# Kernel optimization log

Hardware: AMD Instinct MI355X
Metric: run time of the kernel (lower is better)

The kernel has to match this reference:

```python
import jax, jax.numpy as jnp
import numpy as np

EPS = 1e-6  # flax LayerNorm default

def _layernorm(x, scale, bias):
    mu = jnp.mean(x, axis=-1, keepdims=True)
    var = jnp.mean(jnp.square(x - mu), axis=-1, keepdims=True)
    return (x - mu) * jax.lax.rsqrt(var + EPS) * scale + bias

def _rel_pos_index(ws):
    coords = np.stack(np.meshgrid(np.arange(ws), np.arange(ws), indexing='ij'))  # [2,ws,ws]
    cf = coords.reshape(2, -1)
    rel = (cf[:, :, None] - cf[:, None, :]).transpose(1, 2, 0)  # [N,N,2]
    rel[..., 0] += ws - 1
    rel[..., 1] += ws - 1
    rel[..., 0] *= 2 * ws - 1
    return rel.sum(-1)  # [N,N] in [0,(2ws-1)^2)

def setup_inputs() -> dict:
    key = jax.random.key(0)
    ks = jax.random.split(key, 8)
    B, H, W, C = 16, 56, 56, 384
    L, heads, ws = 2, 12, 7
    s = 0.02
    return {
        'x': jax.random.normal(ks[0], (B, H, W, C), jnp.float32),
        'ln1_s': jnp.ones((L, C), jnp.float32),
        'ln1_b': jnp.zeros((L, C), jnp.float32),
        'qkv_w': jax.random.normal(ks[1], (L, C, 3 * C), jnp.float32) * s,
        'rpb': jax.random.normal(ks[2], (L, (2 * ws - 1) ** 2, heads), jnp.float32) * s,
        'proj_w': jax.random.normal(ks[3], (L, C, C), jnp.float32) * s,
        'ln2_s': jnp.ones((L, C), jnp.float32),
        'ln2_b': jnp.zeros((L, C), jnp.float32),
        'mlp_w1': jax.random.normal(ks[4], (L, C, 4 * C), jnp.float32) * s,
        'mlp_b1': jnp.zeros((L, 4 * C), jnp.float32),
        'mlp_w2': jax.random.normal(ks[5], (L, 4 * C, C), jnp.float32) * s,
        'mlp_b2': jnp.zeros((L, C), jnp.float32),
        'window_size': 7,
    }

def reference(x, ln1_s, ln1_b, qkv_w, rpb, proj_w, ln2_s, ln2_b, mlp_w1, mlp_b1, mlp_w2, mlp_b2, window_size):
    B, H, W, C = x.shape
    ws = int(window_size)
    L = qkv_w.shape[0]
    heads = rpb.shape[-1]
    hd = C // heads
    N = ws * ws
    idx = jnp.asarray(_rel_pos_index(ws))  # [N,N] static

    # --- split to windows: [B,H,W,C] -> [B*nWh*nWw, N, C]
    xw = x.reshape(B, H // ws, ws, W // ws, ws, C)
    xw = xw.transpose(0, 1, 3, 2, 4, 5).reshape(-1, N, C)

    for l in range(L):
        # --- windowed MHSA with relative position bias
        h = _layernorm(xw, ln1_s[l], ln1_b[l])
        qkv = (h @ qkv_w[l]).reshape(-1, N, 3, heads, hd)
        q, k, v = qkv[:, :, 0], qkv[:, :, 1], qkv[:, :, 2]  # [nW,N,heads,hd]
        attn = jnp.einsum('wqhd,wkhd->whqk', q, k) * (hd ** -0.5)
        bias = rpb[l][idx].transpose(2, 0, 1)  # [heads,N,N]
        attn = jax.nn.softmax(attn + bias[None], axis=-1)
        o = jnp.einsum('whqk,wkhd->wqhd', attn, v).reshape(-1, N, C)
        xw = xw + o @ proj_w[l]
        # --- MLP block
        h = _layernorm(xw, ln2_s[l], ln2_b[l])
        h = jax.nn.gelu(h @ mlp_w1[l] + mlp_b1[l])
        xw = xw + (h @ mlp_w2[l] + mlp_b2[l])

    # --- merge windows back to [B,H,W,C]
    out = xw.reshape(B, H // ws, W // ws, ws, ws, C)
    out = out.transpose(0, 1, 3, 2, 4, 5).reshape(B, H, W, C)
    return out
```

## Files before the change

### kernel.cpp

```cpp
#include <hip/hip_runtime.h>
#include <hip/hip_bf16.h>

typedef __bf16 bf16;
typedef __attribute__((ext_vector_type(4))) __bf16 bf16x4;
typedef __attribute__((ext_vector_type(8))) __bf16 bf16x8;
typedef __attribute__((ext_vector_type(4))) float f32x4;

__device__ __forceinline__ void async_ld16(const void* g, void* l) {
    __builtin_amdgcn_global_load_lds(
        (const __attribute__((address_space(1))) unsigned int*)g,
        (__attribute__((address_space(3))) unsigned int*)l, 16, 0, 0);
}

__global__ __launch_bounds__(256) void k_f2bt(const float* __restrict__ in,
                                              bf16* __restrict__ out, int Kd, int Nd) {
    int id = blockIdx.x * 256 + threadIdx.x;
    if (id >= Kd * Nd) return;
    int k = id / Nd, n = id - k * Nd;
    out[(size_t)n * Kd + k] = (bf16)in[id];
}

__global__ __launch_bounds__(256) void k_reorder_in(const float4* __restrict__ x,
                                                    float4* __restrict__ xres) {
    int id = blockIdx.x * 256 + threadIdx.x;
    int c4 = id % 96;
    int t = id / 96;
    int b = t / 3136;
    int rem = t - b * 3136;
    int y = rem / 56;
    int xc = rem - y * 56;
    int w = b * 64 + (y / 7) * 8 + (xc / 7);
    int n = (y % 7) * 7 + (xc % 7);
    xres[(size_t)(w * 49 + n) * 96 + c4] = x[id];
}

__global__ __launch_bounds__(256) void k_reorder_out(const float4* __restrict__ xres,
                                                     float4* __restrict__ out) {
    int id = blockIdx.x * 256 + threadIdx.x;
    int c4 = id % 96;
    int t = id / 96;
    int b = t / 3136;
    int rem = t - b * 3136;
    int y = rem / 56;
    int xc = rem - y * 56;
    int w = b * 64 + (y / 7) * 8 + (xc / 7);
    int n = (y % 7) * 7 + (xc % 7);
    out[id] = xres[(size_t)(w * 49 + n) * 96 + c4];
}

__global__ __launch_bounds__(256) void k_ln(const float* __restrict__ xres,
                                            const float* __restrict__ s,
                                            const float* __restrict__ b,
                                            bf16* __restrict__ h) {
    int t = blockIdx.x * 4 + (threadIdx.x >> 6);
    int lane = threadIdx.x & 63;
    const float4* row = (const float4*)(xres + (size_t)t * 384);
    float4 v0 = row[lane];
    float4 v1 = make_float4(0.f, 0.f, 0.f, 0.f);
    if (lane < 32) v1 = row[64 + lane];
    float sum = v0.x + v0.y + v0.z + v0.w + v1.x + v1.y + v1.z + v1.w;
#pragma unroll
    for (int m = 1; m < 64; m <<= 1) sum += __shfl_xor(sum, m);
    float mu = sum * (1.f / 384.f);
    float sq = (v0.x - mu) * (v0.x - mu) + (v0.y - mu) * (v0.y - mu) +
               (v0.z - mu) * (v0.z - mu) + (v0.w - mu) * (v0.w - mu);
    if (lane < 32)
        sq += (v1.x - mu) * (v1.x - mu) + (v1.y - mu) * (v1.y - mu) +
              (v1.z - mu) * (v1.z - mu) + (v1.w - mu) * (v1.w - mu);
#pragma unroll
    for (int m = 1; m < 64; m <<= 1) sq += __shfl_xor(sq, m);
    float r = rsqrtf(sq * (1.f / 384.f) + 1e-6f);
    const float4* s4 = (const float4*)s;
    const float4* b4 = (const float4*)b;
    bf16* ho = h + (size_t)t * 384;
    {
        float4 sv = s4[lane], bv = b4[lane];
        bf16x4 ov;
        ov[0] = (bf16)((v0.x - mu) * r * sv.x + bv.x);
        ov[1] = (bf16)((v0.y - mu) * r * sv.y + bv.y);
        ov[2] = (bf16)((v0.z - mu) * r * sv.z + bv.z);
        ov[3] = (bf16)((v0.w - mu) * r * sv.w + bv.w);
        *(bf16x4*)&ho[lane * 4] = ov;
    }
    if (lane < 32) {
        float4 sv = s4[64 + lane], bv = b4[64 + lane];
        bf16x4 ov;
        ov[0] = (bf16)((v1.x - mu) * r * sv.x + bv.x);
        ov[1] = (bf16)((v1.y - mu) * r * sv.y + bv.y);
        ov[2] = (bf16)((v1.z - mu) * r * sv.z + bv.z);
        ov[3] = (bf16)((v1.w - mu) * r * sv.w + bv.w);
        *(bf16x4*)&ho[256 + lane * 4] = ov;
    }
}

__device__ inline float gelu_f(float x) {
    float u = 0.7978845608028654f * (x + 0.044715f * x * x * x);
    float t = 1.f - 2.f / (__expf(2.f * u) + 1.f);
    return 0.5f * x * (1.f + t);
}

template <int EPI>
__global__ __launch_bounds__(256) void k_gemm(const bf16* __restrict__ A,
                                              const bf16* __restrict__ Bt,
                                              const float* __restrict__ bias,
                                              float* __restrict__ resid,
                                              bf16* __restrict__ Cout,
                                              int N, int K) {
    __shared__ __align__(16) bf16 As[128 * 64];
    __shared__ __align__(16) bf16 Bs[128 * 64];
    int tid = threadIdx.x;
    int m0 = blockIdx.x * 128;
    int n0 = blockIdx.y * 128;
    int wave = tid >> 6, lane = tid & 63;
    int wm = (wave >> 1) * 64, wn = (wave & 1) * 64;
    int lrow = lane & 15, quad = lane >> 4;

    f32x4 acc[4][4] = {};

    int rsub = lane >> 3;
    int ksl = ((lane & 7) ^ rsub) << 3;
    int rbase = wave * 32 + rsub;
    const bf16* ga = A + (size_t)(m0 + rbase) * K + ksl;
    const bf16* gb = Bt + (size_t)(n0 + rbase) * K + ksl;
    size_t row8 = (size_t)8 * K;
    bf16* lA = &As[wave * 32 * 64];
    bf16* lB = &Bs[wave * 32 * 64];

    for (int kb = 0; kb < K; kb += 64) {
        __syncthreads();
#pragma unroll
        for (int c = 0; c < 4; c++) {
            async_ld16(ga + c * row8 + kb, lA + c * 512);
            async_ld16(gb + c * row8 + kb, lB + c * 512);
        }
        __syncthreads();

        bf16x8 af[2][4], bfv[2][4];
#pragma unroll
        for (int kk = 0; kk < 2; kk++) {
#pragma unroll
            for (int i = 0; i < 4; i++) {
                int ra = wm + i * 16 + lrow;
                af[kk][i] = *(const bf16x8*)&As[ra * 64 + (((kk * 4 + quad) ^ (ra & 7)) << 3)];
                int rb = wn + i * 16 + lrow;
                bfv[kk][i] = *(const bf16x8*)&Bs[rb * 64 + (((kk * 4 + quad) ^ (rb & 7)) << 3)];
            }
        }
#pragma unroll
        for (int kk = 0; kk < 2; kk++)
#pragma unroll
            for (int mi = 0; mi < 4; mi++)
#pragma unroll
                for (int ni = 0; ni < 4; ni++)
                    acc[mi][ni] = __builtin_amdgcn_mfma_f32_16x16x32_bf16(
                        af[kk][mi], bfv[kk][ni], acc[mi][ni], 0, 0, 0);
    }

#pragma unroll
    for (int mi = 0; mi < 4; mi++) {
#pragma unroll
        for (int ni = 0; ni < 4; ni++) {
            int gn = n0 + wn + ni * 16 + lrow;
            float bv = 0.f;
            if (EPI == 1 || EPI == 3) bv = bias[gn];
#pragma unroll
            for (int r = 0; r < 4; r++) {
                int gm = m0 + wm + mi * 16 + quad * 4 + r;
                size_t off = (size_t)gm * N + gn;
                float val = acc[mi][ni][r];
                if (EPI == 0) {
                    Cout[off] = (bf16)val;
                } else if (EPI == 1) {
                    Cout[off] = (bf16)gelu_f(val + bv);
                } else if (EPI == 2) {
                    resid[off] += val;
                } else {
                    resid[off] += val + bv;
                }
            }
        }
    }
}

__global__ __launch_bounds__(256) void k_attn(const bf16* __restrict__ qkv,
                                              const float* __restrict__ rpb,
                                              bf16* __restrict__ o) {
    __shared__ unsigned short relIdx[2401];
    __shared__ float rpbs[4][169];
    __shared__ __align__(16) bf16 Vs[4][32 * 72];
    __shared__ __align__(16) bf16 Ps[4][64 * 72];

    int tid = threadIdx.x;
    int wave = tid >> 6, lane = tid & 63;
    int col = lane & 15, quad = lane >> 4;
    int w = blockIdx.x;
    int head = blockIdx.y * 4 + wave;
    const float scale = 0.17677669529663687f;

    for (int e = tid; e < 2401; e += 256) {
        int i = e / 49, j = e - i * 49;
        int yi = i / 7, xi = i - yi * 7, yj = j / 7, xj = j - yj * 7;
        relIdx[e] = (unsigned short)((yi - yj + 6) * 13 + (xi - xj + 6));
    }
    for (int e = lane; e < 169; e += 64) rpbs[wave][e] = rpb[e * 12 + head];

    const bf16* base = qkv + (size_t)w * 49 * 1152 + head * 32;
    bf16* vsw = Vs[wave];
    bf16* psw = Ps[wave];

    bf16x4 z4 = {(bf16)0.f, (bf16)0.f, (bf16)0.f, (bf16)0.f};
    for (int e = lane; e < 576; e += 64) *(bf16x4*)&vsw[e * 4] = z4;
    for (int e = lane; e < 392; e += 64) {
        int j = e >> 3, d4 = (e & 7) * 4;
        bf16x4 vv = *(const bf16x4*)&base[768 + (size_t)j * 1152 + d4];
        vsw[(d4 + 0) * 72 + j] = vv[0];
        vsw[(d4 + 1) * 72 + j] = vv[1];
        vsw[(d4 + 2) * 72 + j] = vv[2];
        vsw[(d4 + 3) * 72 + j] = vv[3];
    }

    __syncthreads();

    bf16x8 qf[4], kf[4];
#pragma unroll
    for (int mi = 0; mi < 4; mi++) {
        size_t row = (size_t)(mi * 16 + col) * 1152 + quad * 8;
        qf[mi] = *(const bf16x8*)&base[row];
        kf[mi] = *(const bf16x8*)&base[384 + row];
    }

    f32x4 S[4][4] = {};
#pragma unroll
    for (int mi = 0; mi < 4; mi++)
#pragma unroll
        for (int nj = 0; nj < 4; nj++)
            S[mi][nj] = __builtin_amdgcn_mfma_f32_16x16x32_bf16(qf[mi], kf[nj], S[mi][nj], 0, 0, 0);

    float* rp = rpbs[wave];
#pragma unroll
    for (int mi = 0; mi < 4; mi++) {
#pragma unroll
        for (int r = 0; r < 4; r++) {
            int ii = mi * 16 + quad * 4 + r;
            int ir = (ii < 49 ? ii : 0) * 49;
            float sv[4];
            float mx = -1e30f;
#pragma unroll
            for (int nj = 0; nj < 4; nj++) {
                int j = nj * 16 + col;
                float v;
                if (j < 49) v = S[mi][nj][r] * scale + rp[relIdx[ir + j]];
                else v = -1e30f;
                sv[nj] = v;
                mx = fmaxf(mx, v);
            }
#pragma unroll
            for (int m = 1; m < 16; m <<= 1) mx = fmaxf(mx, __shfl_xor(mx, m));
            float sum = 0.f;
#pragma unroll
            for (int nj = 0; nj < 4; nj++) {
                float p = __expf(sv[nj] - mx);
                sv[nj] = p;
                sum += p;
            }
#pragma unroll
            for (int m = 1; m < 16; m <<= 1) sum += __shfl_xor(sum, m);
            float is = 1.f / sum;
#pragma unroll
            for (int nj = 0; nj < 4; nj++)
                psw[ii * 72 + nj * 16 + col] = (bf16)(sv[nj] * is);
        }
    }

    __syncthreads();

    f32x4 O[4][2] = {};
#pragma unroll
    for (int kt = 0; kt < 2; kt++) {
        bf16x8 vb[2];
#pragma unroll
        for (int nt = 0; nt < 2; nt++)
            vb[nt] = *(const bf16x8*)&vsw[(nt * 16 + col) * 72 + kt * 32 + quad * 8];
#pragma unroll
        for (int mi = 0; mi < 4; mi++) {
            bf16x8 pa = *(const bf16x8*)&psw[(mi * 16 + col) * 72 + kt * 32 + quad * 8];
#pragma unroll
            for (int nt = 0; nt < 2; nt++)
                O[mi][nt] = __builtin_amdgcn_mfma_f32_16x16x32_bf16(pa, vb[nt], O[mi][nt], 0, 0, 0);
        }
    }

    bf16* ob = o + (size_t)w * 49 * 384 + head * 32;
#pragma unroll
    for (int mi = 0; mi < 4; mi++) {
#pragma unroll
        for (int r = 0; r < 4; r++) {
            int i = mi * 16 + quad * 4 + r;
            if (i < 49) {
#pragma unroll
                for (int nt = 0; nt < 2; nt++)
                    ob[(size_t)i * 384 + nt * 16 + col] = (bf16)O[mi][nt][r];
            }
        }
    }
}

extern "C" void kernel_launch(void* const* d_in, const int* in_sizes, int n_in,
                              void* d_out, int out_size, void* d_ws, size_t ws_size,
                              hipStream_t stream) {
    const float* x      = (const float*)d_in[0];
    const float* ln1_s  = (const float*)d_in[1];
    const float* ln1_b  = (const float*)d_in[2];
    const float* qkv_w  = (const float*)d_in[3];
    const float* rpb    = (const float*)d_in[4];
    const float* proj_w = (const float*)d_in[5];
    const float* ln2_s  = (const float*)d_in[6];
    const float* ln2_b  = (const float*)d_in[7];
    const float* mlp_w1 = (const float*)d_in[8];
    const float* mlp_b1 = (const float*)d_in[9];
    const float* mlp_w2 = (const float*)d_in[10];
    const float* mlp_b2 = (const float*)d_in[11];
    float* out = (float*)d_out;

    char* ws = (char*)d_ws;
    float* xres  = (float*)ws;
    bf16* qkvbuf = (bf16*)(ws + 77070336);
    bf16* obuf   = (bf16*)(ws + 192675840);
    bf16* wbuf   = (bf16*)(ws + 231211008);
    bf16* hidden = qkvbuf;
    bf16* hbuf   = (bf16*)d_out;

    bf16* qkvw_b  = wbuf;
    bf16* projw_b = wbuf + 884736;
    bf16* mlp1_b  = wbuf + 1179648;
    bf16* mlp2_b  = wbuf + 2359296;

    for (int l = 0; l < 2; l++) {
        k_f2bt<<<1728, 256, 0, stream>>>(qkv_w + (size_t)l * 442368,
                                         qkvw_b + (size_t)l * 442368, 384, 1152);
        k_f2bt<<<576, 256, 0, stream>>>(proj_w + (size_t)l * 147456,
                                        projw_b + (size_t)l * 147456, 384, 384);
        k_f2bt<<<2304, 256, 0, stream>>>(mlp_w1 + (size_t)l * 589824,
                                         mlp1_b + (size_t)l * 589824, 384, 1536);
        k_f2bt<<<2304, 256, 0, stream>>>(mlp_w2 + (size_t)l * 589824,
                                         mlp2_b + (size_t)l * 589824, 1536, 384);
    }

    k_reorder_in<<<18816, 256, 0, stream>>>((const float4*)x, (float4*)xres);

    for (int l = 0; l < 2; l++) {
        k_ln<<<12544, 256, 0, stream>>>(xres, ln1_s + l * 384, ln1_b + l * 384, hbuf);
        k_gemm<0><<<dim3(392, 9), 256, 0, stream>>>(
            hbuf, qkvw_b + (size_t)l * 442368, nullptr, nullptr, qkvbuf, 1152, 384);
        k_attn<<<dim3(1024, 3), 256, 0, stream>>>(qkvbuf, rpb + l * 169 * 12, obuf);
        k_gemm<2><<<dim3(392, 3), 256, 0, stream>>>(
            obuf, projw_b + (size_t)l * 147456, nullptr, xres, nullptr, 384, 384);
        k_ln<<<12544, 256, 0, stream>>>(xres, ln2_s + l * 384, ln2_b + l * 384, hbuf);
        k_gemm<1><<<dim3(392, 12), 256, 0, stream>>>(
            hbuf, mlp1_b + (size_t)l * 589824, mlp_b1 + l * 1536, nullptr, hidden, 1536, 384);
        k_gemm<3><<<dim3(392, 3), 256, 0, stream>>>(
            hidden, mlp2_b + (size_t)l * 589824, mlp_b2 + l * 384, xres, nullptr, 384, 1536);
    }

    k_reorder_out<<<18816, 256, 0, stream>>>((const float4*)xres, (float4*)out);
}
```

Measured before the change: 1.311 ms.

## Stage GEMM epilogue through LDS for vectorized stores and swap grid order

```diff
diff --git a/kernel.cpp b/kernel.cpp
--- a/kernel.cpp
+++ b/kernel.cpp
@@ -106,77 +106,105 @@
                                               float* __restrict__ resid,
                                               bf16* __restrict__ Cout,
                                               int N, int K) {
-    __shared__ __align__(16) bf16 As[128 * 64];
-    __shared__ __align__(16) bf16 Bs[128 * 64];
+    __shared__ __align__(16) char lds[17408];
+    bf16* As = (bf16*)lds;
+    bf16* Bs = (bf16*)(lds + 8192);
     int tid = threadIdx.x;
-    int m0 = blockIdx.x * 128;
-    int n0 = blockIdx.y * 128;
+    int n0 = blockIdx.x * 128;
+    int m0 = blockIdx.y * 128;
     int wave = tid >> 6, lane = tid & 63;
     int wm = (wave >> 1) * 64, wn = (wave & 1) * 64;
-    int lrow = lane & 15, quad = lane >> 4;
+    int col = lane & 15, quad = lane >> 4;
 
     f32x4 acc[4][4] = {};
 
-    int rsub = lane >> 3;
-    int ksl = ((lane & 7) ^ rsub) << 3;
-    int rbase = wave * 32 + rsub;
-    const bf16* ga = A + (size_t)(m0 + rbase) * K + ksl;
-    const bf16* gb = Bt + (size_t)(n0 + rbase) * K + ksl;
-    size_t row8 = (size_t)8 * K;
-    bf16* lA = &As[wave * 32 * 64];
-    bf16* lB = &Bs[wave * 32 * 64];
-
-    for (int kb = 0; kb < K; kb += 64) {
+    int r0 = 2 * wave * 16 + (lane >> 2);
+    int ksl = (lane & 3) ^ ((r0 >> 1) & 3);
+    const bf16* ga0 = A + (size_t)(m0 + r0) * K + ksl * 8;
+    const bf16* gb0 = Bt + (size_t)(n0 + r0) * K + ksl * 8;
+    size_t rowK16 = (size_t)16 * K;
+    bf16* la0 = &As[2 * wave * 512];
+    bf16* la1 = &As[(2 * wave + 1) * 512];
+    bf16* lb0 = &Bs[2 * wave * 512];
+    bf16* lb1 = &Bs[(2 * wave + 1) * 512];
+
+    for (int kb = 0; kb < K; kb += 32) {
         __syncthreads();
-#pragma unroll
-        for (int c = 0; c < 4; c++) {
-            async_ld16(ga + c * row8 + kb, lA + c * 512);
-            async_ld16(gb + c * row8 + kb, lB + c * 512);
-        }
+        async_ld16(ga0 + kb, la0);
+        async_ld16(ga0 + rowK16 + kb, la1);
+        async_ld16(gb0 + kb, lb0);
+        async_ld16(gb0 + rowK16 + kb, lb1);
         __syncthreads();
 
-        bf16x8 af[2][4], bfv[2][4];
-#pragma unroll
-        for (int kk = 0; kk < 2; kk++) {
-#pragma unroll
-            for (int i = 0; i < 4; i++) {
-                int ra = wm + i * 16 + lrow;
-                af[kk][i] = *(const bf16x8*)&As[ra * 64 + (((kk * 4 + quad) ^ (ra & 7)) << 3)];
-                int rb = wn + i * 16 + lrow;
-                bfv[kk][i] = *(const bf16x8*)&Bs[rb * 64 + (((kk * 4 + quad) ^ (rb & 7)) << 3)];
-            }
-        }
-#pragma unroll
-        for (int kk = 0; kk < 2; kk++)
-#pragma unroll
-            for (int mi = 0; mi < 4; mi++)
-#pragma unroll
-                for (int ni = 0; ni < 4; ni++)
-                    acc[mi][ni] = __builtin_amdgcn_mfma_f32_16x16x32_bf16(
-                        af[kk][mi], bfv[kk][ni], acc[mi][ni], 0, 0, 0);
-    }
-
+        bf16x8 af[4], bfv[4];
+#pragma unroll
+        for (int i = 0; i < 4; i++) {
+            int ra = wm + i * 16 + col;
+            af[i] = *(const bf16x8*)&As[ra * 32 + ((quad ^ ((ra >> 1) & 3)) << 3)];
+            int rb = wn + i * 16 + col;
+            bfv[i] = *(const bf16x8*)&Bs[rb * 32 + ((quad ^ ((rb >> 1) & 3)) << 3)];
+        }
+#pragma unroll
+        for (int mi = 0; mi < 4; mi++)
+#pragma unroll
+            for (int ni = 0; ni < 4; ni++)
+                acc[mi][ni] = __builtin_amdgcn_mfma_f32_16x16x32_bf16(
+                    af[mi], bfv[ni], acc[mi][ni], 0, 0, 0);
+    }
+
+    __syncthreads();
+    float* scrw = (float*)lds + wave * (16 * 68);
+
+    int prow = lane >> 3;
+    int pc0 = (lane & 7) * 8;
 #pragma unroll
     for (int mi = 0; mi < 4; mi++) {
 #pragma unroll
-        for (int ni = 0; ni < 4; ni++) {
-            int gn = n0 + wn + ni * 16 + lrow;
-            float bv = 0.f;
-            if (EPI == 1 || EPI == 3) bv = bias[gn];
-#pragma unroll
-            for (int r = 0; r < 4; r++) {
-                int gm = m0 + wm + mi * 16 + quad * 4 + r;
-                size_t off = (size_t)gm * N + gn;
-                float val = acc[mi][ni][r];
-                if (EPI == 0) {
-                    Cout[off] = (bf16)val;
-                } else if (EPI == 1) {
-                    Cout[off] = (bf16)gelu_f(val + bv);
-                } else if (EPI == 2) {
-                    resid[off] += val;
-                } else {
-                    resid[off] += val + bv;
-                }
+        for (int ni = 0; ni < 4; ni++)
+#pragma unroll
+            for (int r = 0; r < 4; r++)
+                scrw[(quad * 4 + r) * 68 + ni * 16 + col] = acc[mi][ni][r];
+#pragma unroll
+        for (int h = 0; h < 2; h++) {
+            int lr = h * 8 + prow;
+            const float* sp = scrw + lr * 68 + pc0;
+            float4 u0 = *(const float4*)sp;
+            float4 u1 = *(const float4*)(sp + 4);
+            int gm = m0 + wm + mi * 16 + lr;
+            int gn = n0 + wn + pc0;
+            size_t off = (size_t)gm * N + gn;
+            if (EPI == 0) {
+                bf16x8 ov;
+                ov[0] = (bf16)u0.x; ov[1] = (bf16)u0.y; ov[2] = (bf16)u0.z; ov[3] = (bf16)u0.w;
+                ov[4] = (bf16)u1.x; ov[5] = (bf16)u1.y; ov[6] = (bf16)u1.z; ov[7] = (bf16)u1.w;
+                *(bf16x8*)&Cout[off] = ov;
+            } else if (EPI == 1) {
+                float4 b0 = *(const float4*)&bias[gn];
+                float4 b1 = *(const float4*)&bias[gn + 4];
+                bf16x8 ov;
+                ov[0] = (bf16)gelu_f(u0.x + b0.x); ov[1] = (bf16)gelu_f(u0.y + b0.y);
+                ov[2] = (bf16)gelu_f(u0.z + b0.z); ov[3] = (bf16)gelu_f(u0.w + b0.w);
+                ov[4] = (bf16)gelu_f(u1.x + b1.x); ov[5] = (bf16)gelu_f(u1.y + b1.y);
+                ov[6] = (bf16)gelu_f(u1.z + b1.z); ov[7] = (bf16)gelu_f(u1.w + b1.w);
+                *(bf16x8*)&Cout[off] = ov;
+            } else if (EPI == 2) {
+                float4 r0v = *(const float4*)&resid[off];
+                float4 r1v = *(const float4*)&resid[off + 4];
+                r0v.x += u0.x; r0v.y += u0.y; r0v.z += u0.z; r0v.w += u0.w;
+                r1v.x += u1.x; r1v.y += u1.y; r1v.z += u1.z; r1v.w += u1.w;
+                *(float4*)&resid[off] = r0v;
+                *(float4*)&resid[off + 4] = r1v;
+            } else {
+                float4 b0 = *(const float4*)&bias[gn];
+                float4 b1 = *(const float4*)&bias[gn + 4];
+                float4 r0v = *(const float4*)&resid[off];
+                float4 r1v = *(const float4*)&resid[off + 4];
+                r0v.x += u0.x + b0.x; r0v.y += u0.y + b0.y;
+                r0v.z += u0.z + b0.z; r0v.w += u0.w + b0.w;
+                r1v.x += u1.x + b1.x; r1v.y += u1.y + b1.y;
+                r1v.z += u1.z + b1.z; r1v.w += u1.w + b1.w;
+                *(float4*)&resid[off] = r0v;
+                *(float4*)&resid[off + 4] = r1v;
             }
         }
     }
@@ -350,15 +378,15 @@
 
     for (int l = 0; l < 2; l++) {
         k_ln<<<12544, 256, 0, stream>>>(xres, ln1_s + l * 384, ln1_b + l * 384, hbuf);
-        k_gemm<0><<<dim3(392, 9), 256, 0, stream>>>(
+        k_gemm<0><<<dim3(9, 392), 256, 0, stream>>>(
             hbuf, qkvw_b + (size_t)l * 442368, nullptr, nullptr, qkvbuf, 1152, 384);
         k_attn<<<dim3(1024, 3), 256, 0, stream>>>(qkvbuf, rpb + l * 169 * 12, obuf);
-        k_gemm<2><<<dim3(392, 3), 256, 0, stream>>>(
+        k_gemm<2><<<dim3(3, 392), 256, 0, stream>>>(
             obuf, projw_b + (size_t)l * 147456, nullptr, xres, nullptr, 384, 384);
         k_ln<<<12544, 256, 0, stream>>>(xres, ln2_s + l * 384, ln2_b + l * 384, hbuf);
-        k_gemm<1><<<dim3(392, 12), 256, 0, stream>>>(
+        k_gemm<1><<<dim3(12, 392), 256, 0, stream>>>(
             hbuf, mlp1_b + (size_t)l * 589824, mlp_b1 + l * 1536, nullptr, hidden, 1536, 384);
-        k_gemm<3><<<dim3(392, 3), 256, 0, stream>>>(
+        k_gemm<3><<<dim3(3, 392), 256, 0, stream>>>(
             hidden, mlp2_b + (size_t)l * 589824, mlp_b2 + l * 384, xres, nullptr, 384, 1536);
     }
 
```

Result: faster. 1.248 ms (-4.9%).
